# Performance work log

Hardware: AMD Instinct MI355X
Metric: run time of the kernel (lower is better)

Reference implementation:

```python
import jax, jax.numpy as jnp
import numpy as np

N = 100_000      # nodes
E = 1_600_000    # edges
F_IN = 128       # n_features == conv_dim1..3
F_OUT = 256      # concat_dim
G = 2000         # number of graphs in the batch
EPS = 1e-5       # BatchNorm eps


def _xavier(k, shape):
    fan_in, fan_out = shape[-2], shape[-1]
    lim = float(np.sqrt(6.0 / (fan_in + fan_out)))
    return jax.random.uniform(k, shape, jnp.float32, -lim, lim)


def setup_inputs() -> dict:
    key = jax.random.key(0)
    ks = jax.random.split(key, 8)
    x = jax.random.normal(ks[0], (N, F_IN), jnp.float32)
    edge_index = jax.random.randint(ks[1], (2, E), 0, N, dtype=jnp.int64)
    batch = jnp.sort(jax.random.randint(ks[2], (N,), 0, G, dtype=jnp.int64))
    # layers 1..5: F_IN -> F_IN (stacked), layer 6: F_IN -> F_OUT
    Wi = _xavier(ks[3], (5, F_IN, F_IN))   # ARMA init_weight per layer
    Wr = _xavier(ks[4], (5, F_IN, F_IN))   # ARMA root_weight per layer
    b = jnp.zeros((5, F_IN), jnp.float32)  # ARMA bias per layer
    g = jnp.ones((5, F_IN), jnp.float32)   # BN gamma
    be = jnp.zeros((5, F_IN), jnp.float32) # BN beta
    Wi6 = _xavier(ks[5], (F_IN, F_OUT))
    Wr6 = _xavier(ks[6], (F_IN, F_OUT))
    b6 = jnp.zeros((F_OUT,), jnp.float32)
    g6 = jnp.ones((F_OUT,), jnp.float32)
    be6 = jnp.zeros((F_OUT,), jnp.float32)
    return dict(x=x, edge_index=edge_index, batch=batch, Wi=Wi, Wr=Wr, b=b,
                g=g, be=be, Wi6=Wi6, Wr6=Wr6, b6=b6, g6=g6, be6=be6)


def _arma(x, norm, row, col, Wi_l, Wr_l, b_l):
    # ARMAConv (num_stacks=1, num_layers=1, act=ReLU):
    #   out = ReLU( A_norm @ (x W_init) + x W_root + b )
    h = x @ Wi_l                                           # [N, F_out]
    msg = h[row] * norm[:, None]                           # gather + scale, [E, F_out]
    agg = jax.ops.segment_sum(msg, col, num_segments=N)    # scatter-add
    return jax.nn.relu(agg + x @ Wr_l + b_l)


def _bn(x, gamma, beta):
    # BatchNorm1d, training mode (biased batch variance)
    mu = x.mean(axis=0)
    var = x.var(axis=0)
    return gamma * (x - mu) * jax.lax.rsqrt(var + EPS) + beta


def reference(x, edge_index, batch, Wi, Wr, b, g, be, Wi6, Wr6, b6, g6, be6):
    row, col = edge_index[0], edge_index[1]
    # gcn_norm without self loops: D^-1/2 A D^-1/2 edge weights
    deg = jax.ops.segment_sum(jnp.ones((E,), x.dtype), col, num_segments=N)
    dinv = jnp.where(deg > 0, jax.lax.rsqrt(deg), 0.0)
    norm = dinv[row] * dinv[col]                           # [E]

    h = x
    for l in range(5):  # fixed small layer count
        h = _arma(h, norm, row, col, Wi[l], Wr[l], b[l])   # outer F.relu is idempotent
        h = _bn(h, g[l], be[l])
    h = _arma(h, norm, row, col, Wi6, Wr6, b6)
    h = _bn(h, g6, be6)
    # global_add_pool over graph ids; dropout = identity (deterministic baseline)
    out = jax.ops.segment_sum(h, batch, num_segments=G)    # [G, F_OUT]
    return out
```

## Files before the change

### kernel.cpp

```cpp
#include <hip/hip_runtime.h>

#define Nn 100000
#define NP 100001
#define Ee 1600000
#define Gg 2000
#define EPSf 1e-5f

typedef unsigned short ushort_t;
typedef __attribute__((ext_vector_type(8))) short short8;
typedef __attribute__((ext_vector_type(4))) float f32x4;
typedef __attribute__((ext_vector_type(4))) unsigned u32x4;

__device__ inline float bf2f(unsigned int u) {
    union { unsigned int i; float f; } v; v.i = u << 16; return v.f;
}
__device__ inline unsigned short f2bf(float f) {
    unsigned int x = __float_as_uint(f);
    unsigned int r = (x + 0x7fffu + ((x >> 16) & 1u)) >> 16;
    return (unsigned short)r;
}
__device__ inline int ldidx(const void* a, int i, int i64) {
    return i64 ? (int)((const long long*)a)[i] : ((const int*)a)[i];
}
__device__ inline float ldflt(const void* p, long long i, int f32) {
    return f32 ? ((const float*)p)[i] : bf2f(((const ushort_t*)p)[i]);
}


__global__ void k_flags(const void* gones, const void* ei, int* flags) {
    if (threadIdx.x == 0 && blockIdx.x == 0) {
        unsigned w = *(const unsigned*)gones;
        flags[0] = (w == 0x3F800000u) ? 1 : 0;
        const int* e = (const int*)ei;
        int nz = 0;
        for (int i = 0; i < 256; i++) nz |= e[2 * i + 1];
        flags[1] = nz ? 0 : 1;
    }
}


__global__ void k_hist(const void* __restrict__ ei, int* __restrict__ deg, const int* __restrict__ flags) {
    int i = blockIdx.x * 256 + threadIdx.x;
    if (i < Ee) {
        int c = ldidx(ei, Ee + i, flags[1]);
        atomicAdd(&deg[c], 1);
    }
}

__global__ void k_dinv(const int* __restrict__ deg, float* __restrict__ dinv) {
    int i = blockIdx.x * 256 + threadIdx.x;
    if (i < Nn) { int d = deg[i]; dinv[i] = d > 0 ? rsqrtf((float)d) : 0.f; }
}

__global__ void k_scan1(const int* __restrict__ deg, int* __restrict__ off, int* __restrict__ part) {
    __shared__ int sh[1024];
    int i = blockIdx.x * 1024 + threadIdx.x;
    int v = (i < Nn) ? ((deg[i] + 3) & ~3) : 0;
    sh[threadIdx.x] = v;
    __syncthreads();
    for (int ofs = 1; ofs < 1024; ofs <<= 1) {
        int t = 0;
        if ((int)threadIdx.x >= ofs) t = sh[threadIdx.x - ofs];
        __syncthreads();
        sh[threadIdx.x] += t;
        __syncthreads();
    }
    if (i < Nn) off[i] = sh[threadIdx.x] - v;
    if (threadIdx.x == 1023) part[blockIdx.x] = sh[1023];
}

__global__ void k_scan2(int* part, int nb) {
    if (threadIdx.x == 0 && blockIdx.x == 0) {
        int run = 0;
        for (int i = 0; i < nb; i++) { int t = part[i]; part[i] = run; run += t; }
        part[nb] = run;
    }
}

__global__ void k_scan3(int* __restrict__ off, const int* __restrict__ part, int* __restrict__ cursor) {
    int i = blockIdx.x * 256 + threadIdx.x;
    if (i < Nn) {
        int v = off[i] + part[i >> 10];
        off[i] = v;
        cursor[i] = v;
    }
    if (i == 0) off[Nn] = part[98];
}

__global__ void k_fillp(const void* __restrict__ ei, int* __restrict__ cursor,
                        int* __restrict__ srcS, const int* __restrict__ flags) {
    int range = blockIdx.x & 7;
    int e = (blockIdx.x >> 3) * 256 + threadIdx.x;
    if (e < Ee) {
        int i64 = flags[1];
        int c = ldidx(ei, Ee + e, i64);
        if (c >= range * 12500 && c < (range + 1) * 12500) {
            int r = ldidx(ei, e, i64);
            int p = atomicAdd(&cursor[c], 1);
            srcS[p] = r;
        }
    }
}

__global__ void k_pad(const int* __restrict__ cursor, const int* __restrict__ off,
                      int* __restrict__ srcS) {
    int i = blockIdx.x * 256 + threadIdx.x;
    if (i < Nn) {
        int e = off[i + 1];
        for (int p = cursor[i]; p < e; p++) srcS[p] = Nn;
    }
}

__global__ void k_zrow(ushort_t* __restrict__ Hi) {
    int t = threadIdx.x;
    int fc = t >> 4, j = t & 15;
    Hi[((size_t)fc * NP + Nn) * 16 + j] = 0;
}

__global__ void k_cvtp(const void* b, const void* b6, const void* g, const void* g6,
                       const void* be, const void* be6,
                       float* __restrict__ biasF, float* __restrict__ gF,
                       float* __restrict__ beF, const int* __restrict__ flags) {
    int i = blockIdx.x * 256 + threadIdx.x;
    if (i >= 2688) return;
    int grp = i / 896, r = i - grp * 896;
    int f32 = flags[0];
    const void* srcs[6] = { b, b6, g, g6, be, be6 };
    float* dsts[3] = { biasF, gF, beF };
    const void* s = (r < 640) ? srcs[grp * 2] : srcs[grp * 2 + 1];
    int idx = (r < 640) ? r : r - 640;
    dsts[grp][r] = ldflt(s, idx, f32);
}

__global__ void k_cvtx(const void* __restrict__ x, ushort_t* __restrict__ xq, const int* __restrict__ flags) {
    int node = blockIdx.x * 256 + threadIdx.x;
    int fc = blockIdx.y;
    if (node < Nn) {
        union { ushort_t u[16]; u32x4 v[2]; } t;
        if (flags[0]) {
            const float* p = (const float*)x + (size_t)node * 128 + fc * 16;
#pragma unroll
            for (int j = 0; j < 16; j++) t.u[j] = f2bf(p[j]);
        } else {
            const ushort_t* p = (const ushort_t*)x + (size_t)node * 128 + fc * 16;
#pragma unroll
            for (int j = 0; j < 16; j++) t.u[j] = p[j];
        }
        u32x4* d = (u32x4*)(xq + ((size_t)fc * Nn + node) * 16);
        d[0] = t.v[0]; d[1] = t.v[1];
    }
}

__global__ void k_pack(const void* __restrict__ Wi, const void* __restrict__ Wr,
                       const void* __restrict__ Wi6, const void* __restrict__ Wr6,
                       ushort_t* __restrict__ Bp, const int* __restrict__ flags) {
    int idx = blockIdx.x * 256 + threadIdx.x;
    if (idx >= 229376) return;
    int f32 = flags[0];
    if (idx < 163840) {
        int l = idx / 32768, rem = idx - l * 32768;
        int kg = rem / 2048, rem2 = rem - kg * 2048;
        int n = rem2 / 8, j = rem2 - n * 8;
        int k = kg * 8 + j;
        float v = (n < 128) ? ldflt(Wi, (l * 128 + k) * 128 + n, f32)
                            : ldflt(Wr, (l * 128 + k) * 128 + (n - 128), f32);
        Bp[idx] = f2bf(v);
    } else {
        int idx2 = idx - 163840;
        int kg = idx2 / 4096, rem2 = idx2 - kg * 4096;
        int n = rem2 / 8, j = rem2 - n * 8;
        int k = kg * 8 + j;
        float v = (n < 256) ? ldflt(Wi6, k * 256 + n, f32) : ldflt(Wr6, k * 256 + (n - 256), f32);
        Bp[idx] = f2bf(v);
    }
}

__global__ void k_fold(const ushort_t* __restrict__ Bp, const float* __restrict__ stat,
                       const float* __restrict__ gamma, const float* __restrict__ beta,
                       const float* __restrict__ bias,
                       ushort_t* __restrict__ Bp2, float* __restrict__ hcorr, int ncat) {
    __shared__ float red[128];
    int n = blockIdx.x, k = threadIdx.x;
    int fhalf = ncat >> 1;
    float mu = stat[k] * (1.f / Nn);
    float var = stat[128 + k] * (1.f / Nn) - mu * mu;
    float rs = rsqrtf(var + EPSf);
    float s = gamma[k] * rs;
    float h = beta[k] - s * mu;
    size_t idx = ((size_t)(k >> 3) * ncat + n) * 8 + (k & 7);
    float w = bf2f(Bp[idx]);
    Bp2[idx] = f2bf(w * s);
    red[k] = h * w;
    __syncthreads();
    for (int m = 64; m > 0; m >>= 1) { if (k < m) red[k] += red[k + m]; __syncthreads(); }
    if (k == 0) hcorr[n] = red[0] + (n >= fhalf ? bias[n - fhalf] : 0.f);
}

__global__ void k_h0(const float* __restrict__ bias, float* __restrict__ hc, int ncat) {
    int n = blockIdx.x * 256 + threadIdx.x;
    if (n < ncat) hc[n] = n >= (ncat >> 1) ? bias[n - (ncat >> 1)] : 0.f;
}


__global__ __launch_bounds__(256) void k_gemm(
        const ushort_t* __restrict__ Aq,
        const ushort_t* __restrict__ Bp, const float* __restrict__ hcorr,
        const float* __restrict__ dinv,
        ushort_t* __restrict__ Hi, ushort_t* __restrict__ yq, int ncat) {
    __shared__ ushort_t stage[32 * 264];
    const int tid = threadIdx.x, lane = tid & 63, wid = tid >> 6;
    const int q = lane >> 4, l15 = lane & 15;
    const int fhalf = ncat >> 1;
    const int colW = blockIdx.y * 256 + wid * 64;
    const int row0 = blockIdx.x * 64;

    short8 bfr[4][4];
    float hc[4];
#pragma unroll
    for (int kk = 0; kk < 4; kk++) {
        int kg = kk * 4 + q;
#pragma unroll
        for (int ct = 0; ct < 4; ct++)
            bfr[kk][ct] = *(const short8*)(Bp + ((size_t)kg * ncat + colW + ct * 16 + l15) * 8);
    }
#pragma unroll
    for (int ct = 0; ct < 4; ct++) hc[ct] = hcorr[colW + ct * 16 + l15];

    f32x4 acc[4][4];
    f32x4 z; z.x = 0.f; z.y = 0.f; z.z = 0.f; z.w = 0.f;
#pragma unroll
    for (int rt = 0; rt < 4; rt++)
#pragma unroll
        for (int ct = 0; ct < 4; ct++) acc[rt][ct] = z;

#pragma unroll
    for (int kk = 0; kk < 4; kk++) {
        int kg = kk * 4 + q;
        const ushort_t* ap = Aq + (size_t)(kg >> 1) * Nn * 16 + (kg & 1) * 8;
        short8 af[4];
#pragma unroll
        for (int rt = 0; rt < 4; rt++) {
            int node = row0 + rt * 16 + l15;
            if (node >= Nn) node = Nn - 1;
            af[rt] = *(const short8*)(ap + (size_t)node * 16);
        }
#pragma unroll
        for (int rt = 0; rt < 4; rt++)
#pragma unroll
            for (int ct = 0; ct < 4; ct++)
                acc[rt][ct] = __builtin_amdgcn_mfma_f32_16x16x32_bf16(af[rt], bfr[kk][ct], acc[rt][ct], 0, 0, 0);
    }

#pragma unroll
    for (int half = 0; half < 2; half++) {
        __syncthreads();
#pragma unroll
        for (int ct = 0; ct < 4; ct++) {
            int lcol = wid * 64 + ct * 16 + l15;
            bool isHi = (blockIdx.y * 256 + lcol) < fhalf;
#pragma unroll
            for (int rt2 = 0; rt2 < 2; rt2++) {
                int rt = half * 2 + rt2;
#pragma unroll
                for (int r = 0; r < 4; r++) {
                    int grow = row0 + rt * 16 + q * 4 + r;
                    int gr = grow < Nn ? grow : 0;
                    float v = acc[rt][ct][r] + hc[ct];
                    if (isHi) v *= dinv[gr];
                    stage[(rt2 * 16 + q * 4 + r) * 264 + lcol] = f2bf(v);
                }
            }
        }
        __syncthreads();
        for (int chunk = tid; chunk < 512; chunk += 256) {
            int cg = chunk & 15, rl = chunk >> 4;
            int node = row0 + half * 32 + rl;
            if (node < Nn) {
                int gc0 = blockIdx.y * 256 + cg * 16;
                const u32x4* sp = (const u32x4*)&stage[rl * 264 + cg * 16];
                u32x4 v0 = sp[0], v1 = sp[1];
                ushort_t* dst = (gc0 < fhalf)
                    ? Hi + ((size_t)(gc0 >> 4) * NP + node) * 16
                    : yq + ((size_t)((gc0 - fhalf) >> 4) * Nn + node) * 16;
                u32x4* dp = (u32x4*)dst;
                dp[0] = v0; dp[1] = v1;
            }
        }
    }
}


__global__ __launch_bounds__(256) void k_agg8(const int* __restrict__ off, const int* __restrict__ src,
                                              const float* __restrict__ dinv, const unsigned* __restrict__ Hi2,
                                              unsigned* __restrict__ yq, float* __restrict__ stat,
                                              int F, int fcbase) {
    const int tid = threadIdx.x;
    const int w = tid >> 6, lane = tid & 63;
    const int sub = lane >> 3, fl = lane & 7;
    const int fc = fcbase + (blockIdx.x & 7);
    const int T = blockIdx.x >> 3;
    const unsigned* __restrict__ base = Hi2 + (size_t)fc * (NP * 8) + fl;
    float st0 = 0.f, st1 = 0.f, st2 = 0.f, st3 = 0.f;

#pragma unroll
    for (int pass = 0; pass < 4; pass++) {
        int node = T * 128 + pass * 32 + w * 8 + sub;
        bool valid = node < Nn;
        int p0 = 0, p1 = 0;
        if (valid) { p0 = off[node]; p1 = off[node + 1]; }
        float a0 = 0.f, a1 = 0.f;
        int p = p0;
        for (; p + 15 < p1; p += 16) {
            int4 sa = *(const int4*)(src + p);
            int4 sb = *(const int4*)(src + p + 4);
            int4 sc = *(const int4*)(src + p + 8);
            int4 sd = *(const int4*)(src + p + 12);
            unsigned u0 = base[(unsigned)sa.x * 8u];
            unsigned u1 = base[(unsigned)sa.y * 8u];
            unsigned u2 = base[(unsigned)sa.z * 8u];
            unsigned u3 = base[(unsigned)sa.w * 8u];
            unsigned u4 = base[(unsigned)sb.x * 8u];
            unsigned u5 = base[(unsigned)sb.y * 8u];
            unsigned u6 = base[(unsigned)sb.z * 8u];
            unsigned u7 = base[(unsigned)sb.w * 8u];
            unsigned u8 = base[(unsigned)sc.x * 8u];
            unsigned u9 = base[(unsigned)sc.y * 8u];
            unsigned uA = base[(unsigned)sc.z * 8u];
            unsigned uB = base[(unsigned)sc.w * 8u];
            unsigned uC = base[(unsigned)sd.x * 8u];
            unsigned uD = base[(unsigned)sd.y * 8u];
            unsigned uE = base[(unsigned)sd.z * 8u];
            unsigned uF = base[(unsigned)sd.w * 8u];
            a0 += bf2f(u0 & 0xffffu); a1 += bf2f(u0 >> 16);
            a0 += bf2f(u1 & 0xffffu); a1 += bf2f(u1 >> 16);
            a0 += bf2f(u2 & 0xffffu); a1 += bf2f(u2 >> 16);
            a0 += bf2f(u3 & 0xffffu); a1 += bf2f(u3 >> 16);
            a0 += bf2f(u4 & 0xffffu); a1 += bf2f(u4 >> 16);
            a0 += bf2f(u5 & 0xffffu); a1 += bf2f(u5 >> 16);
            a0 += bf2f(u6 & 0xffffu); a1 += bf2f(u6 >> 16);
            a0 += bf2f(u7 & 0xffffu); a1 += bf2f(u7 >> 16);
            a0 += bf2f(u8 & 0xffffu); a1 += bf2f(u8 >> 16);
            a0 += bf2f(u9 & 0xffffu); a1 += bf2f(u9 >> 16);
            a0 += bf2f(uA & 0xffffu); a1 += bf2f(uA >> 16);
            a0 += bf2f(uB & 0xffffu); a1 += bf2f(uB >> 16);
            a0 += bf2f(uC & 0xffffu); a1 += bf2f(uC >> 16);
            a0 += bf2f(uD & 0xffffu); a1 += bf2f(uD >> 16);
            a0 += bf2f(uE & 0xffffu); a1 += bf2f(uE >> 16);
            a0 += bf2f(uF & 0xffffu); a1 += bf2f(uF >> 16);
        }
        for (; p + 7 < p1; p += 8) {
            int4 sa = *(const int4*)(src + p);
            int4 sb = *(const int4*)(src + p + 4);
            unsigned u0 = base[(unsigned)sa.x * 8u];
            unsigned u1 = base[(unsigned)sa.y * 8u];
            unsigned u2 = base[(unsigned)sa.z * 8u];
            unsigned u3 = base[(unsigned)sa.w * 8u];
            unsigned u4 = base[(unsigned)sb.x * 8u];
            unsigned u5 = base[(unsigned)sb.y * 8u];
            unsigned u6 = base[(unsigned)sb.z * 8u];
            unsigned u7 = base[(unsigned)sb.w * 8u];
            a0 += bf2f(u0 & 0xffffu); a1 += bf2f(u0 >> 16);
            a0 += bf2f(u1 & 0xffffu); a1 += bf2f(u1 >> 16);
            a0 += bf2f(u2 & 0xffffu); a1 += bf2f(u2 >> 16);
            a0 += bf2f(u3 & 0xffffu); a1 += bf2f(u3 >> 16);
            a0 += bf2f(u4 & 0xffffu); a1 += bf2f(u4 >> 16);
            a0 += bf2f(u5 & 0xffffu); a1 += bf2f(u5 >> 16);
            a0 += bf2f(u6 & 0xffffu); a1 += bf2f(u6 >> 16);
            a0 += bf2f(u7 & 0xffffu); a1 += bf2f(u7 >> 16);
        }
        if (p < p1) {
            int4 sa = *(const int4*)(src + p);
            unsigned u0 = base[(unsigned)sa.x * 8u];
            unsigned u1 = base[(unsigned)sa.y * 8u];
            unsigned u2 = base[(unsigned)sa.z * 8u];
            unsigned u3 = base[(unsigned)sa.w * 8u];
            a0 += bf2f(u0 & 0xffffu); a1 += bf2f(u0 >> 16);
            a0 += bf2f(u1 & 0xffffu); a1 += bf2f(u1 >> 16);
            a0 += bf2f(u2 & 0xffffu); a1 += bf2f(u2 >> 16);
            a0 += bf2f(u3 & 0xffffu); a1 += bf2f(u3 >> 16);
        }
        if (valid) {
            float dv = dinv[node];
            unsigned* yp = yq + ((size_t)fc * Nn + node) * 8 + fl;
            unsigned uv = *yp;
            float vx = fmaxf(bf2f(uv & 0xffffu) + dv * a0, 0.f);
            float vy = fmaxf(bf2f(uv >> 16) + dv * a1, 0.f);
            *yp = (unsigned)f2bf(vx) | ((unsigned)f2bf(vy) << 16);
            st0 += vx; st1 += vx * vx;
            st2 += vy; st3 += vy * vy;
        }
    }
#pragma unroll
    for (int m = 8; m <= 32; m <<= 1) {
        st0 += __shfl_xor(st0, m, 64);
        st1 += __shfl_xor(st1, m, 64);
        st2 += __shfl_xor(st2, m, 64);
        st3 += __shfl_xor(st3, m, 64);
    }
    __shared__ float red[4][8][4];
    if (sub == 0) {
        red[w][fl][0] = st0; red[w][fl][1] = st1;
        red[w][fl][2] = st2; red[w][fl][3] = st3;
    }
    __syncthreads();
    if (tid < 32) {
        int rfl = tid >> 2, k = tid & 3;
        float s = red[0][rfl][k] + red[1][rfl][k] + red[2][rfl][k] + red[3][rfl][k];
        int f = fc * 16 + rfl * 2 + (k >> 1);
        atomicAdd(&stat[(k & 1) * F + f], s);
    }
}


__device__ inline int lb(const void* a, int n, int key, int i64) {
    int lo = 0, hi = n;
    while (lo < hi) { int mid = (lo + hi) >> 1; if (ldidx(a, mid, i64) < key) lo = mid + 1; else hi = mid; }
    return lo;
}

__global__ void k_pool(const ushort_t* __restrict__ y6q, const float* __restrict__ stat,
                       const float* __restrict__ g6, const float* __restrict__ be6,
                       const void* __restrict__ batch, void* __restrict__ out,
                       const int* __restrict__ flags) {
    int g = blockIdx.x;
    int f = threadIdx.x;
    int i64 = flags[1];
    int start = lb(batch, Nn, g, i64);
    int end = lb(batch, Nn, g + 1, i64);
    const ushort_t* yp = y6q + (size_t)(f >> 4) * Nn * 16 + (f & 15);
    float s = 0.f;
    for (int n = start; n < end; n++) s += bf2f(yp[(size_t)n * 16]);
    int cnt = end - start;
    float mu = stat[f] * (1.f / Nn);
    float var = stat[256 + f] * (1.f / Nn) - mu * mu;
    float rs = rsqrtf(var + EPSf);
    float val = g6[f] * rs * (s - (float)cnt * mu) + (float)cnt * be6[f];
    if (flags[0]) ((float*)out)[(size_t)g * 256 + f] = val;
    else          ((ushort_t*)out)[(size_t)g * 256 + f] = f2bf(val);
}


extern "C" void kernel_launch(void* const* d_in, const int* in_sizes, int n_in,
                              void* d_out, int out_size, void* d_ws, size_t ws_size,
                              hipStream_t stream) {
    const void* x    = d_in[0];
    const void* ei   = d_in[1];
    const void* batch= d_in[2];
    const void* Wi   = d_in[3];
    const void* Wr   = d_in[4];
    const void* b    = d_in[5];
    const void* g    = d_in[6];
    const void* be   = d_in[7];
    const void* Wi6  = d_in[8];
    const void* Wr6  = d_in[9];
    const void* b6   = d_in[10];
    const void* g6   = d_in[11];
    const void* be6  = d_in[12];

    char* p = (char*)d_ws;
    auto alloc = [&](size_t bytes) { char* r = p; p += (bytes + 511) & ~(size_t)511; return r; };
    ushort_t* HiB  = (ushort_t*)alloc((size_t)NP * 256 * 2);
    ushort_t* xq   = (ushort_t*)alloc((size_t)Nn * 128 * 2);
    ushort_t* yAq  = (ushort_t*)alloc((size_t)Nn * 128 * 2);
    ushort_t* yBq  = (ushort_t*)alloc((size_t)Nn * 128 * 2);
    ushort_t* y6q  = (ushort_t*)alloc((size_t)Nn * 256 * 2);
    int* srcS      = (int*)alloc(((size_t)Ee + 4 * Nn + 64) * 4);
    int* off       = (int*)alloc((size_t)(Nn + 1) * 4);
    int* cursor    = (int*)alloc((size_t)Nn * 4);
    int* deg       = (int*)alloc((size_t)Nn * 4);
    float* dinv    = (float*)alloc((size_t)Nn * 4);
    int* part      = (int*)alloc(128 * 4);
    float* statsA  = (float*)alloc(6 * 512 * 4);
    ushort_t* Bp   = (ushort_t*)alloc(229376 * 2);
    ushort_t* Bp2  = (ushort_t*)alloc(65536 * 2);
    float* hcorrA  = (float*)alloc(512 * 4);
    int* flags     = (int*)alloc(2 * 4);
    float* biasF   = (float*)alloc(896 * 4);
    float* gF      = (float*)alloc(896 * 4);
    float* beF     = (float*)alloc(896 * 4);
    const unsigned* Hi2 = (const unsigned*)HiB;

    const int AGG_GRID = 782 * 8;
    const int GEMM_GRID = 1563;

    k_flags<<<1, 64, 0, stream>>>(g, ei, flags);
    k_cvtp<<<11, 256, 0, stream>>>(b, b6, g, g6, be, be6, biasF, gF, beF, flags);

    hipMemsetAsync(deg, 0, (size_t)Nn * 4, stream);
    hipMemsetAsync(statsA, 0, 6 * 512 * 4, stream);
    k_hist<<<6250, 256, 0, stream>>>(ei, deg, flags);
    k_dinv<<<391, 256, 0, stream>>>(deg, dinv);
    k_scan1<<<98, 1024, 0, stream>>>(deg, off, part);
    k_scan2<<<1, 64, 0, stream>>>(part, 98);
    k_scan3<<<391, 256, 0, stream>>>(off, part, cursor);
    k_fillp<<<50000, 256, 0, stream>>>(ei, cursor, srcS, flags);
    k_pad<<<391, 256, 0, stream>>>(cursor, off, srcS);
    k_zrow<<<1, 256, 0, stream>>>(HiB);
    k_pack<<<896, 256, 0, stream>>>(Wi, Wr, Wi6, Wr6, Bp, flags);
    k_cvtx<<<dim3(391, 8), 256, 0, stream>>>(x, xq, flags);
    k_h0<<<1, 256, 0, stream>>>(biasF, hcorrA, 256);

    k_gemm<<<dim3(GEMM_GRID, 1), 256, 0, stream>>>(xq, Bp, hcorrA, dinv, HiB, yAq, 256);
    k_agg8<<<AGG_GRID, 256, 0, stream>>>(off, srcS, dinv, Hi2, (unsigned*)yAq, statsA, 128, 0);
    k_fold<<<256, 128, 0, stream>>>(Bp + 32768, statsA, gF, beF, biasF + 128, Bp2, hcorrA, 256);

    k_gemm<<<dim3(GEMM_GRID, 1), 256, 0, stream>>>(yAq, Bp2, hcorrA, dinv, HiB, yBq, 256);
    k_agg8<<<AGG_GRID, 256, 0, stream>>>(off, srcS, dinv, Hi2, (unsigned*)yBq, statsA + 512, 128, 0);
    k_fold<<<256, 128, 0, stream>>>(Bp + 65536, statsA + 512, gF + 128, beF + 128, biasF + 256, Bp2, hcorrA, 256);

    k_gemm<<<dim3(GEMM_GRID, 1), 256, 0, stream>>>(yBq, Bp2, hcorrA, dinv, HiB, yAq, 256);
    k_agg8<<<AGG_GRID, 256, 0, stream>>>(off, srcS, dinv, Hi2, (unsigned*)yAq, statsA + 1024, 128, 0);
    k_fold<<<256, 128, 0, stream>>>(Bp + 98304, statsA + 1024, gF + 256, beF + 256, biasF + 384, Bp2, hcorrA, 256);

    k_gemm<<<dim3(GEMM_GRID, 1), 256, 0, stream>>>(yAq, Bp2, hcorrA, dinv, HiB, yBq, 256);
    k_agg8<<<AGG_GRID, 256, 0, stream>>>(off, srcS, dinv, Hi2, (unsigned*)yBq, statsA + 1536, 128, 0);
    k_fold<<<256, 128, 0, stream>>>(Bp + 131072, statsA + 1536, gF + 384, beF + 384, biasF + 512, Bp2, hcorrA, 256);

    k_gemm<<<dim3(GEMM_GRID, 1), 256, 0, stream>>>(yBq, Bp2, hcorrA, dinv, HiB, yAq, 256);
    k_agg8<<<AGG_GRID, 256, 0, stream>>>(off, srcS, dinv, Hi2, (unsigned*)yAq, statsA + 2048, 128, 0);
    k_fold<<<512, 128, 0, stream>>>(Bp + 163840, statsA + 2048, gF + 512, beF + 512, biasF + 640, Bp2, hcorrA, 512);

    k_gemm<<<dim3(GEMM_GRID, 2), 256, 0, stream>>>(yAq, Bp2, hcorrA, dinv, HiB, y6q, 512);
    k_agg8<<<AGG_GRID, 256, 0, stream>>>(off, srcS, dinv, Hi2, (unsigned*)y6q, statsA + 2560, 256, 0);
    k_agg8<<<AGG_GRID, 256, 0, stream>>>(off, srcS, dinv, Hi2, (unsigned*)y6q, statsA + 2560, 256, 8);
    k_pool<<<Gg, 256, 0, stream>>>(y6q, statsA + 2560, gF + 640, beF + 640, batch, d_out, flags);
}
```

Before: 1.149 ms.

## Gather 16-byte feature chunks per lane and split edges across lanes in aggregation

```diff
diff --git a/kernel.cpp b/kernel.cpp
--- a/kernel.cpp
+++ b/kernel.cpp
@@ -297,10 +297,15 @@
     const int tid = threadIdx.x;
     const int w = tid >> 6, lane = tid & 63;
     const int sub = lane >> 3, fl = lane & 7;
+    const int e2 = (fl >> 1) & 3;
+    const int h  = fl & 1;
     const int fc = fcbase + (blockIdx.x & 7);
     const int T = blockIdx.x >> 3;
-    const unsigned* __restrict__ base = Hi2 + (size_t)fc * (NP * 8) + fl;
-    float st0 = 0.f, st1 = 0.f, st2 = 0.f, st3 = 0.f;
+    const char* __restrict__ gbase = (const char*)Hi2 + (size_t)fc * ((size_t)NP * 32) + h * 16;
+
+    float stS[8], stQ[8];
+#pragma unroll
+    for (int j = 0; j < 8; j++) { stS[j] = 0.f; stQ[j] = 0.f; }
 
 #pragma unroll
     for (int pass = 0; pass < 4; pass++) {
@@ -308,106 +313,90 @@
         bool valid = node < Nn;
         int p0 = 0, p1 = 0;
         if (valid) { p0 = off[node]; p1 = off[node + 1]; }
-        float a0 = 0.f, a1 = 0.f;
+        float a[8];
+#pragma unroll
+        for (int j = 0; j < 8; j++) a[j] = 0.f;
         int p = p0;
         for (; p + 15 < p1; p += 16) {
-            int4 sa = *(const int4*)(src + p);
-            int4 sb = *(const int4*)(src + p + 4);
-            int4 sc = *(const int4*)(src + p + 8);
-            int4 sd = *(const int4*)(src + p + 12);
-            unsigned u0 = base[(unsigned)sa.x * 8u];
-            unsigned u1 = base[(unsigned)sa.y * 8u];
-            unsigned u2 = base[(unsigned)sa.z * 8u];
-            unsigned u3 = base[(unsigned)sa.w * 8u];
-            unsigned u4 = base[(unsigned)sb.x * 8u];
-            unsigned u5 = base[(unsigned)sb.y * 8u];
-            unsigned u6 = base[(unsigned)sb.z * 8u];
-            unsigned u7 = base[(unsigned)sb.w * 8u];
-            unsigned u8 = base[(unsigned)sc.x * 8u];
-            unsigned u9 = base[(unsigned)sc.y * 8u];
-            unsigned uA = base[(unsigned)sc.z * 8u];
-            unsigned uB = base[(unsigned)sc.w * 8u];
-            unsigned uC = base[(unsigned)sd.x * 8u];
-            unsigned uD = base[(unsigned)sd.y * 8u];
-            unsigned uE = base[(unsigned)sd.z * 8u];
-            unsigned uF = base[(unsigned)sd.w * 8u];
-            a0 += bf2f(u0 & 0xffffu); a1 += bf2f(u0 >> 16);
-            a0 += bf2f(u1 & 0xffffu); a1 += bf2f(u1 >> 16);
-            a0 += bf2f(u2 & 0xffffu); a1 += bf2f(u2 >> 16);
-            a0 += bf2f(u3 & 0xffffu); a1 += bf2f(u3 >> 16);
-            a0 += bf2f(u4 & 0xffffu); a1 += bf2f(u4 >> 16);
-            a0 += bf2f(u5 & 0xffffu); a1 += bf2f(u5 >> 16);
-            a0 += bf2f(u6 & 0xffffu); a1 += bf2f(u6 >> 16);
-            a0 += bf2f(u7 & 0xffffu); a1 += bf2f(u7 >> 16);
-            a0 += bf2f(u8 & 0xffffu); a1 += bf2f(u8 >> 16);
-            a0 += bf2f(u9 & 0xffffu); a1 += bf2f(u9 >> 16);
-            a0 += bf2f(uA & 0xffffu); a1 += bf2f(uA >> 16);
-            a0 += bf2f(uB & 0xffffu); a1 += bf2f(uB >> 16);
-            a0 += bf2f(uC & 0xffffu); a1 += bf2f(uC >> 16);
-            a0 += bf2f(uD & 0xffffu); a1 += bf2f(uD >> 16);
-            a0 += bf2f(uE & 0xffffu); a1 += bf2f(uE >> 16);
-            a0 += bf2f(uF & 0xffffu); a1 += bf2f(uF >> 16);
-        }
-        for (; p + 7 < p1; p += 8) {
-            int4 sa = *(const int4*)(src + p);
-            int4 sb = *(const int4*)(src + p + 4);
-            unsigned u0 = base[(unsigned)sa.x * 8u];
-            unsigned u1 = base[(unsigned)sa.y * 8u];
-            unsigned u2 = base[(unsigned)sa.z * 8u];
-            unsigned u3 = base[(unsigned)sa.w * 8u];
-            unsigned u4 = base[(unsigned)sb.x * 8u];
-            unsigned u5 = base[(unsigned)sb.y * 8u];
-            unsigned u6 = base[(unsigned)sb.z * 8u];
-            unsigned u7 = base[(unsigned)sb.w * 8u];
-            a0 += bf2f(u0 & 0xffffu); a1 += bf2f(u0 >> 16);
-            a0 += bf2f(u1 & 0xffffu); a1 += bf2f(u1 >> 16);
-            a0 += bf2f(u2 & 0xffffu); a1 += bf2f(u2 >> 16);
-            a0 += bf2f(u3 & 0xffffu); a1 += bf2f(u3 >> 16);
-            a0 += bf2f(u4 & 0xffffu); a1 += bf2f(u4 >> 16);
-            a0 += bf2f(u5 & 0xffffu); a1 += bf2f(u5 >> 16);
-            a0 += bf2f(u6 & 0xffffu); a1 += bf2f(u6 >> 16);
-            a0 += bf2f(u7 & 0xffffu); a1 += bf2f(u7 >> 16);
+            int s0 = src[p + e2];
+            int s1 = src[p + 4 + e2];
+            int s2 = src[p + 8 + e2];
+            int s3 = src[p + 12 + e2];
+            u32x4 g0 = *(const u32x4*)(gbase + (size_t)((unsigned)s0 << 5));
+            u32x4 g1 = *(const u32x4*)(gbase + (size_t)((unsigned)s1 << 5));
+            u32x4 g2 = *(const u32x4*)(gbase + (size_t)((unsigned)s2 << 5));
+            u32x4 g3 = *(const u32x4*)(gbase + (size_t)((unsigned)s3 << 5));
+#pragma unroll
+            for (int d = 0; d < 4; d++) {
+                a[2*d]   += bf2f(g0[d] & 0xffffu); a[2*d+1] += bf2f(g0[d] >> 16);
+                a[2*d]   += bf2f(g1[d] & 0xffffu); a[2*d+1] += bf2f(g1[d] >> 16);
+                a[2*d]   += bf2f(g2[d] & 0xffffu); a[2*d+1] += bf2f(g2[d] >> 16);
+                a[2*d]   += bf2f(g3[d] & 0xffffu); a[2*d+1] += bf2f(g3[d] >> 16);
+            }
+        }
+        if (p + 7 < p1) {
+            int s0 = src[p + e2];
+            int s1 = src[p + 4 + e2];
+            u32x4 g0 = *(const u32x4*)(gbase + (size_t)((unsigned)s0 << 5));
+            u32x4 g1 = *(const u32x4*)(gbase + (size_t)((unsigned)s1 << 5));
+#pragma unroll
+            for (int d = 0; d < 4; d++) {
+                a[2*d]   += bf2f(g0[d] & 0xffffu); a[2*d+1] += bf2f(g0[d] >> 16);
+                a[2*d]   += bf2f(g1[d] & 0xffffu); a[2*d+1] += bf2f(g1[d] >> 16);
+            }
+            p += 8;
         }
         if (p < p1) {
-            int4 sa = *(const int4*)(src + p);
-            unsigned u0 = base[(unsigned)sa.x * 8u];
-            unsigned u1 = base[(unsigned)sa.y * 8u];
-            unsigned u2 = base[(unsigned)sa.z * 8u];
-            unsigned u3 = base[(unsigned)sa.w * 8u];
-            a0 += bf2f(u0 & 0xffffu); a1 += bf2f(u0 >> 16);
-            a0 += bf2f(u1 & 0xffffu); a1 += bf2f(u1 >> 16);
-            a0 += bf2f(u2 & 0xffffu); a1 += bf2f(u2 >> 16);
-            a0 += bf2f(u3 & 0xffffu); a1 += bf2f(u3 >> 16);
-        }
-        if (valid) {
+            int s0 = src[p + e2];
+            u32x4 g0 = *(const u32x4*)(gbase + (size_t)((unsigned)s0 << 5));
+#pragma unroll
+            for (int d = 0; d < 4; d++) {
+                a[2*d]   += bf2f(g0[d] & 0xffffu); a[2*d+1] += bf2f(g0[d] >> 16);
+            }
+        }
+#pragma unroll
+        for (int j = 0; j < 8; j++) {
+            a[j] += __shfl_xor(a[j], 2, 64);
+            a[j] += __shfl_xor(a[j], 4, 64);
+        }
+        if (valid && fl < 2) {
             float dv = dinv[node];
-            unsigned* yp = yq + ((size_t)fc * Nn + node) * 8 + fl;
-            unsigned uv = *yp;
-            float vx = fmaxf(bf2f(uv & 0xffffu) + dv * a0, 0.f);
-            float vy = fmaxf(bf2f(uv >> 16) + dv * a1, 0.f);
-            *yp = (unsigned)f2bf(vx) | ((unsigned)f2bf(vy) << 16);
-            st0 += vx; st1 += vx * vx;
-            st2 += vy; st3 += vy * vy;
-        }
-    }
-#pragma unroll
-    for (int m = 8; m <= 32; m <<= 1) {
-        st0 += __shfl_xor(st0, m, 64);
-        st1 += __shfl_xor(st1, m, 64);
-        st2 += __shfl_xor(st2, m, 64);
-        st3 += __shfl_xor(st3, m, 64);
-    }
-    __shared__ float red[4][8][4];
-    if (sub == 0) {
-        red[w][fl][0] = st0; red[w][fl][1] = st1;
-        red[w][fl][2] = st2; red[w][fl][3] = st3;
+            u32x4* yp = (u32x4*)(yq + ((size_t)fc * Nn + node) * 8 + h * 4);
+            u32x4 uv = *yp;
+#pragma unroll
+            for (int d = 0; d < 4; d++) {
+                float vlo = fmaxf(bf2f(uv[d] & 0xffffu) + dv * a[2*d],   0.f);
+                float vhi = fmaxf(bf2f(uv[d] >> 16)     + dv * a[2*d+1], 0.f);
+                uv[d] = (unsigned)f2bf(vlo) | ((unsigned)f2bf(vhi) << 16);
+                stS[2*d]   += vlo; stQ[2*d]   += vlo * vlo;
+                stS[2*d+1] += vhi; stQ[2*d+1] += vhi * vhi;
+            }
+            *yp = uv;
+        }
+    }
+#pragma unroll
+    for (int j = 0; j < 8; j++) {
+        stS[j] += __shfl_xor(stS[j], 8, 64);
+        stQ[j] += __shfl_xor(stQ[j], 8, 64);
+        stS[j] += __shfl_xor(stS[j], 16, 64);
+        stQ[j] += __shfl_xor(stQ[j], 16, 64);
+        stS[j] += __shfl_xor(stS[j], 32, 64);
+        stQ[j] += __shfl_xor(stQ[j], 32, 64);
+    }
+    __shared__ float red[4][2][8][2];
+    if (lane < 2) {
+#pragma unroll
+        for (int j = 0; j < 8; j++) {
+            red[w][lane][j][0] = stS[j];
+            red[w][lane][j][1] = stQ[j];
+        }
     }
     __syncthreads();
     if (tid < 32) {
-        int rfl = tid >> 2, k = tid & 3;
-        float s = red[0][rfl][k] + red[1][rfl][k] + red[2][rfl][k] + red[3][rfl][k];
-        int f = fc * 16 + rfl * 2 + (k >> 1);
-        atomicAdd(&stat[(k & 1) * F + f], s);
+        int hh = tid >> 4, r = tid & 15, j = r >> 1, m = r & 1;
+        float s = red[0][hh][j][m] + red[1][hh][j][m] + red[2][hh][j][m] + red[3][hh][j][m];
+        int f = fc * 16 + hh * 8 + j;
+        atomicAdd(&stat[m * F + f], s);
     }
 }
 
@@ -523,5 +512,5 @@
     k_gemm<<<dim3(GEMM_GRID, 2), 256, 0, stream>>>(yAq, Bp2, hcorrA, dinv, HiB, y6q, 512);
     k_agg8<<<AGG_GRID, 256, 0, stream>>>(off, srcS, dinv, Hi2, (unsigned*)y6q, statsA + 2560, 256, 0);
     k_agg8<<<AGG_GRID, 256, 0, stream>>>(off, srcS, dinv, Hi2, (unsigned*)y6q, statsA + 2560, 256, 8);
-    k_pool<<<Gg, 256, 0, stream>>>(y6q, statsA + 2560, gF + 640, beF + 640, batch, d_out, flags);
-}
+    k_pool<<<Gg, 256, 0, stream>>>(y6q, statsA + 2560, gF + 640, be6 ? beF + 640 : beF + 640, batch, d_out, flags);
+}
```

After: 1.145 ms. No clear change (-0.4%).
